# Optimization experiments

Measured on AMD Instinct MI355X. Metric: run time of the kernel, lower is better.

Reference implementation:

```python
import jax, jax.numpy as jnp
import numpy as np

# ---- neuron / simulation params (network.yaml analogue) ----
THETA = 10.0      # spike threshold
TAU_SR = 4.0      # SRM (psp) kernel time constant
TAU_REF = 4.0     # refractory kernel time constant
SCALE_REF = 2.0
TS = 1.0          # simulation step
T_SAMPLE = 1000
N_BATCH, N_IN, N_OUT = 16, 2048, 512
SPIKE_RATE = 0.1


def _alpha_kernel(tau, mult, eps_cut):
    # SLAYER _calculateAlphaKernel: truncated alpha function samples
    vals = []
    for t in np.arange(0.0, T_SAMPLE, TS):
        v = mult * t / tau * np.exp(1.0 - t / tau)
        if abs(v) < eps_cut and t > tau:
            break
        vals.append(v)
    return np.asarray(vals, dtype=np.float32)

SRM_KERNEL = _alpha_kernel(TAU_SR, 1.0, 0.01)
REF_KERNEL = _alpha_kernel(TAU_REF, -SCALE_REF * THETA, 0.0001)  # fullRefKernel=True
# pending-refractory shift vector: refKernel[0]==0 is consumed at spike time
REF_SHIFT = jnp.asarray(np.concatenate([REF_KERNEL[1:], [0.0]]).astype(np.float32))


def psp(spike_in):
    # causal temporal filter: psp[n,c,t] = Ts * sum_j srm[j] * s[n,c,t-j]
    N, C, T = spike_in.shape
    Ls = SRM_KERNEL.shape[0]
    x = spike_in.reshape(N * C, 1, T)
    k = jnp.asarray(SRM_KERNEL)[::-1].reshape(1, 1, Ls)  # flip -> convolution
    y = jax.lax.conv_general_dilated(
        x, k, window_strides=(1,), padding=[(Ls - 1, 0)],
        dimension_numbers=('NCH', 'OIH', 'NCH'))
    return y.reshape(N, C, T) * TS


def spike_scan(wpsp):
    # sequential spike generation with refractory feedback (SLAYER getSpikes)
    N, C, T = wpsp.shape
    L = REF_SHIFT.shape[0]

    def step(buf, x):
        u = x + buf[..., 0]                       # membrane incl. past refractory
        ind = (u >= THETA).astype(x.dtype)
        buf = jnp.concatenate([buf[..., 1:], jnp.zeros_like(buf[..., :1])], -1) \
              + ind[..., None] * REF_SHIFT        # schedule refractory for future t
        return buf, (ind / TS, u)

    buf0 = jnp.zeros((N, C, L), wpsp.dtype)
    _, (s, u) = jax.lax.scan(step, buf0, jnp.moveaxis(wpsp, -1, 0))
    return jnp.moveaxis(s, 0, -1), jnp.moveaxis(u, 0, -1)


def setup_inputs() -> dict:
    key = jax.random.key(0)
    k1, k2 = jax.random.split(key)
    spikeInput = (jax.random.uniform(k1, (N_BATCH, N_IN, T_SAMPLE)) < SPIKE_RATE
                  ).astype(jnp.float32)
    weight = jax.random.normal(k2, (N_OUT, N_IN), dtype=jnp.float32) * 0.3
    return {'spikeInput': spikeInput, 'weight': weight}


def reference(spikeInput, weight):
    p = psp(spikeInput)                           # [N, Nin, T]
    wpsp = jnp.einsum('oi,nit->not', weight, p)   # 1x1x1 conv == matmul, no bias
    spikes, _ = spike_scan(wpsp)                  # [N, Nout, T]
    return spikes
```

## Files before the change

### kernel.cpp

```cpp
#include <hip/hip_runtime.h>
#include <hip/hip_bf16.h>
#include <math.h>

#define NB 16
#define NIN 2048
#define NOUT 512
#define TT 1000
#define L_SRM 31

typedef int v4i  __attribute__((ext_vector_type(4)));
typedef int v16i __attribute__((ext_vector_type(16)));

__device__ __forceinline__ unsigned long long spread8(unsigned int b) {
    unsigned long long x = (unsigned long long)(b & 0xFFu) * 0x0101010101010101ULL;
    x &= 0x8040201008040201ULL;
    x |= x >> 4; x |= x >> 2; x |= x >> 1;
    return x & 0x0101010101010101ULL;
}

__global__ __launch_bounds__(256) void k_quant(const float* __restrict__ W,
                                               signed char* __restrict__ Bq) {
    int idx = blockIdx.x * 256 + threadIdx.x;
    int o = idx >> 11, i = idx & (NIN - 1);
    double w = (double)W[o * NIN + i];
    int wq = (int)rint(w * 536870912.0);
    int b0 = (int)(signed char)(wq & 255); int r = (wq - b0) >> 8;
    int b1 = (int)(signed char)(r  & 255); r = (r - b1) >> 8;
    int b2 = (int)(signed char)(r  & 255); r = (r - b2) >> 8;
    int b3 = r;
    size_t e = (size_t)o * NIN + i;
    Bq[e]                = (signed char)b0;
    Bq[e + 1048576]      = (signed char)b1;
    Bq[e + 2097152]      = (signed char)b2;
    Bq[e + 3145728]      = (signed char)b3;
}

__global__ __launch_bounds__(256) void k_extract(const float* __restrict__ s,
                                                 unsigned long long* __restrict__ bits) {
    __shared__ float tile[64][65];
    int tc = blockIdx.x, ic = blockIdx.y, n = blockIdx.z;
    int t0 = tc * 64, i0 = ic * 64;
    int tid = threadIdx.x;
    int r = tid >> 2, cq = tid & 3;
    const float* rp = s + ((size_t)(n * NIN + i0 + r)) * TT + t0;
    #pragma unroll
    for (int q = 0; q < 4; ++q) {
        int col = cq * 16 + q * 4;
        float4 v = make_float4(0.f, 0.f, 0.f, 0.f);
        if (t0 + col + 3 < TT) v = *(const float4*)(rp + col);
        tile[r][col] = v.x; tile[r][col + 1] = v.y;
        tile[r][col + 2] = v.z; tile[r][col + 3] = v.w;
    }
    __syncthreads();
    int lane = tid & 63, w = tid >> 6;
    #pragma unroll
    for (int k = 0; k < 16; ++k) {
        int tl = w * 16 + k;
        if (t0 + tl >= TT) break;
        unsigned long long m = __ballot(tile[lane][tl] != 0.0f);
        if (lane == 0) bits[((size_t)n * TT + t0 + tl) * 32 + ic] = m;
    }
}

__global__ __launch_bounds__(512) void k_spmm(const unsigned long long* __restrict__ bits,
                                              const signed char* __restrict__ Bq,
                                              double* __restrict__ z) {
    __shared__ char Alds[128 * 128];
    __shared__ char Blds[4][64 * 128];
    int tid = threadIdx.x;
    int bid = blockIdx.x;
    int o0  = (bid & 7) * 64;
    int nt0 = (bid >> 3) * 128;

    const int arow_w = tid >> 2, q = tid & 3;
    const int p_st = tid >> 7, orow = (tid >> 1) & 63, h = tid & 1;
    const unsigned int* agp = (const unsigned int*)bits + (size_t)(nt0 + arow_w) * 64 + q;
    const signed char*  bgp = Bq + (size_t)p_st * (NOUT * NIN)
                                 + (size_t)(o0 + orow) * NIN + h * 64;
    char* awp = Alds + arow_w * 128;
    const int xra_w = arow_w & 7;
    char* bwp = Blds[p_st] + orow * 128;
    const int xro_w = orow & 7;

    const int l = tid & 63, wv = tid >> 6;
    const int wm = wv >> 1, wn = wv & 1;
    const int arow = wm * 32 + (l & 31), xra = arow & 7;
    const int brow = wn * 32 + (l & 31), xrb = brow & 7;
    const int kg = l >> 5;

    v16i acc0 = {}, acc1 = {}, acc2 = {}, acc3 = {};

    unsigned int aw = agp[0];
    int4 bs0 = ((const int4*)bgp)[0], bs1 = ((const int4*)bgp)[1],
         bs2 = ((const int4*)bgp)[2], bs3 = ((const int4*)bgp)[3];

    for (int ks = 0; ks < 16; ++ks) {
        __syncthreads();
        {
            unsigned long long s0 = spread8(aw), s1 = spread8(aw >> 8),
                               s2 = spread8(aw >> 16), s3 = spread8(aw >> 24);
            ulonglong2 v0; v0.x = s0; v0.y = s1;
            ulonglong2 v1; v1.x = s2; v1.y = s3;
            *(ulonglong2*)(awp + (((2 * q)     ^ xra_w) << 4)) = v0;
            *(ulonglong2*)(awp + (((2 * q + 1) ^ xra_w) << 4)) = v1;
            *(int4*)(bwp + (((h * 4 + 0) ^ xro_w) << 4)) = bs0;
            *(int4*)(bwp + (((h * 4 + 1) ^ xro_w) << 4)) = bs1;
            *(int4*)(bwp + (((h * 4 + 2) ^ xro_w) << 4)) = bs2;
            *(int4*)(bwp + (((h * 4 + 3) ^ xro_w) << 4)) = bs3;
        }
        __syncthreads();
        if (ks < 15) {
            aw = agp[(ks + 1) * 4];
            const int4* g = (const int4*)(bgp + (size_t)(ks + 1) * 128);
            bs0 = g[0]; bs1 = g[1]; bs2 = g[2]; bs3 = g[3];
        }
        #pragma unroll
        for (int ksub = 0; ksub < 4; ++ksub) {
            int ca = ksub * 2 + kg;
            v4i av  = *(const v4i*)(Alds    + arow * 128 + (((ca) ^ xra) << 4));
            v4i bv0 = *(const v4i*)(Blds[0] + brow * 128 + (((ca) ^ xrb) << 4));
            v4i bv1 = *(const v4i*)(Blds[1] + brow * 128 + (((ca) ^ xrb) << 4));
            v4i bv2 = *(const v4i*)(Blds[2] + brow * 128 + (((ca) ^ xrb) << 4));
            v4i bv3 = *(const v4i*)(Blds[3] + brow * 128 + (((ca) ^ xrb) << 4));
            acc0 = __builtin_amdgcn_mfma_i32_32x32x32_i8(av, bv0, acc0, 0, 0, 0);
            acc1 = __builtin_amdgcn_mfma_i32_32x32x32_i8(av, bv1, acc1, 0, 0, 0);
            acc2 = __builtin_amdgcn_mfma_i32_32x32x32_i8(av, bv2, acc2, 0, 0, 0);
            acc3 = __builtin_amdgcn_mfma_i32_32x32x32_i8(av, bv3, acc3, 0, 0, 0);
        }
    }

    #pragma unroll
    for (int r = 0; r < 16; ++r) {
        int row = (r & 3) + 8 * (r >> 2) + 4 * kg;
        long long tot = ((long long)acc3[r] << 24) + ((long long)acc2[r] << 16)
                      + ((long long)acc1[r] << 8)  +  (long long)acc0[r];
        double zv = (double)tot * (1.0 / 536870912.0);
        __builtin_nontemporal_store(zv,
            &z[(size_t)(nt0 + wm * 32 + row) * NOUT + (o0 + wn * 32 + (l & 31))]);
    }
}

__global__ __launch_bounds__(128) void k_conv(const double* __restrict__ z,
                                              double* __restrict__ wpsp) {
    __shared__ float srm_s[32];
    __shared__ __align__(16) double zs[62 * 128];
    int tid = threadIdx.x;
    if (tid < L_SRM) {
        double t = (double)tid;
        srm_s[tid] = (float)((t / 4.0) * exp(1.0 - t / 4.0));
    }
    int tb = blockIdx.x * 32;
    int oc = blockIdx.y * 128;
    int n  = blockIdx.z;
    const double* zp = z + ((size_t)n * TT) * NOUT + oc;
    int wv = tid >> 6, lane = tid & 63;
    for (int r = wv; r < 62; r += 2) {
        int t = tb - 30 + r;
        if (t >= 0 && t < TT) {
            const double* src = zp + (size_t)t * NOUT + lane * 2;
            __builtin_amdgcn_global_load_lds(
                (const __attribute__((address_space(1))) void*)src,
                (__attribute__((address_space(3))) void*)(&zs[r * 128]),
                16, 0, 0);
        } else {
            double2 zero; zero.x = 0.0; zero.y = 0.0;
            *(double2*)(&zs[r * 128 + lane * 2]) = zero;
        }
    }
    asm volatile("s_waitcnt vmcnt(0)" ::: "memory");
    __syncthreads();
    for (int tl = 0; tl < 32; ++tl) {
        int t = tb + tl;
        if (t >= TT) break;
        double a0 = 0., a1 = 0., a2 = 0., a3 = 0.;
        #pragma unroll
        for (int jj = 0; jj < 28; jj += 4) {
            a0 += (double)srm_s[jj]     * zs[(tl + 30 - jj) * 128 + tid];
            a1 += (double)srm_s[jj + 1] * zs[(tl + 29 - jj) * 128 + tid];
            a2 += (double)srm_s[jj + 2] * zs[(tl + 28 - jj) * 128 + tid];
            a3 += (double)srm_s[jj + 3] * zs[(tl + 27 - jj) * 128 + tid];
        }
        a0 += (double)srm_s[28] * zs[(tl + 2) * 128 + tid];
        a1 += (double)srm_s[29] * zs[(tl + 1) * 128 + tid];
        a2 += (double)srm_s[30] * zs[(tl + 0) * 128 + tid];
        wpsp[((size_t)n * TT + t) * NOUT + oc + tid] = (a0 + a1) + (a2 + a3);
    }
}

__global__ __launch_bounds__(64) void k_scan(const double* __restrict__ wpsp,
                                             float* __restrict__ out) {
    __shared__ float  refTab[64];
    __shared__ double Tb[8][256];
    __shared__ __align__(16) double xbuf[2][33 * 64];
    __shared__ float  obuf[64 * 33];
    int lane = threadIdx.x;
    {
        double d = (double)lane;
        refTab[lane] = (lane == 0) ? 0.0f
                     : (float)(-20.0 * (d / 4.0) * exp(1.0 - d / 4.0));
    }
    __syncthreads();
    for (int e = lane; e < 2048; e += 64) {
        int k = e >> 8, m = e & 255;
        double s = 0.0;
        #pragma unroll
        for (int j = 0; j < 8; ++j) {
            int idx = 8 * k + j + 1;
            if (((m >> j) & 1) && idx <= 63) s += (double)refTab[idx];
        }
        Tb[k][m] = s;
    }

    int n  = blockIdx.x >> 3;
    int o0 = (blockIdx.x & 7) << 6;
    const double* wp = wpsp + ((size_t)n * TT) * NOUT + o0;
    float* op = out + ((size_t)(n * NOUT) + o0 + lane) * TT;

    int halfSel = lane >> 5;
    int colSel  = (lane & 31) * 2;
    #define STAGE(bf, tb, nrows)                                                   \
        for (int p = 0; p < (nrows) / 2; ++p) {                                    \
            const double* src = wp + (size_t)((tb) + 2 * p + halfSel) * NOUT + colSel; \
            __builtin_amdgcn_global_load_lds(                                      \
                (const __attribute__((address_space(1))) void*)src,                \
                (__attribute__((address_space(3))) void*)(&xbuf[bf][p * 128]),     \
                16, 0, 0);                                                         \
        }

    unsigned long long hist = 0ULL;
    bool sp = false;
    int buf = 0;
    STAGE(0, 0, 32);
    asm volatile("s_waitcnt vmcnt(0)" ::: "memory");
    __syncthreads();

    double x = xbuf[0][lane];
    double partial = 0.0;
    double c0 = 0.0, c1 = Tb[0][1];

    for (int tb = 0; tb < TT; tb += 32) {
        int nnext = TT - (tb + 32); if (nnext > 32) nnext = 32;
        if (nnext > 0) { STAGE(buf ^ 1, tb + 32, nnext); }
        #pragma unroll
        for (int tl = 0; tl < 32; ++tl) {
            hist = ((hist << 1) | (unsigned long long)sp) & 0x7FFFFFFFFFFFFFFFULL;
            unsigned long long hs = (hist << 1) & 0x7FFFFFFFFFFFFFFFULL;
            double T1 = Tb[1][(unsigned)((hs >>  8) & 255)];
            double T2 = Tb[2][(unsigned)((hs >> 16) & 255)];
            double T3 = Tb[3][(unsigned)((hs >> 24) & 255)];
            double T4 = Tb[4][(unsigned)((hs >> 32) & 255)];
            double T5 = Tb[5][(unsigned)((hs >> 40) & 255)];
            double T6 = Tb[6][(unsigned)((hs >> 48) & 255)];
            double T7 = Tb[7][(unsigned)((hs >> 56) & 255)];
            unsigned m = (unsigned)(hs & 255);
            double nc0 = Tb[0][m];
            double nc1 = Tb[0][m | 1];
            double nx  = xbuf[buf][(tl + 1) * 64 + lane];
            double u = (x + partial) + (sp ? c1 : c0);
            sp = (u >= 10.0);
            obuf[lane * 33 + tl] = sp ? 1.0f : 0.0f;
            partial = ((T1 + T2) + (T3 + T4)) + ((T5 + T6) + T7);
            c0 = nc0; c1 = nc1; x = nx;
        }
        int nrows = TT - tb; if (nrows > 32) nrows = 32;
        for (int k = 0; k + 3 < nrows; k += 4) {
            float4 v = make_float4(obuf[lane * 33 + k],     obuf[lane * 33 + k + 1],
                                   obuf[lane * 33 + k + 2], obuf[lane * 33 + k + 3]);
            *(float4*)(op + tb + k) = v;
        }
        asm volatile("s_waitcnt vmcnt(0)" ::: "memory");
        __syncthreads();
        buf ^= 1;
        x = xbuf[buf][lane];
    }
    #undef STAGE
}

extern "C" void kernel_launch(void* const* d_in, const int* in_sizes, int n_in,
                              void* d_out, int out_size, void* d_ws, size_t ws_size,
                              hipStream_t stream) {
    const float* spikeInput = (const float*)d_in[0];
    const float* weight     = (const float*)d_in[1];
    float* out = (float*)d_out;

    char* ws = (char*)d_ws;
    unsigned long long* bits = (unsigned long long*)ws;
    signed char*        Bq   = (signed char*)(ws + 4194304);
    double*             z    = (double*)(ws + 8388608);
    double*             wpsp = (double*)(ws + 73924608);

    k_quant<<<(NOUT * NIN) / 256, 256, 0, stream>>>(weight, Bq);
    k_extract<<<dim3(16, 32, 16), 256, 0, stream>>>(spikeInput, bits);
    k_spmm<<<1000, 512, 0, stream>>>(bits, Bq, z);
    k_conv<<<dim3(32, 4, 16), 128, 0, stream>>>(z, wpsp);
    k_scan<<<128, 64, 0, stream>>>(wpsp, out);
}
```

Before: 485.6 us.

## Pipeline spike scan recurrence two steps ahead to shorten critical path

The sequential spike-scan loop now computes refractory partial sums and the next membrane input one step further ahead. This leaves only an add, a compare and a select on the per-timestep dependency chain, which the serial scan is bound by. The lookup-table entries for the next step are fetched as paired double2 loads, and the input staging buffer grows by one row to allow the deeper lookahead. The cost is more live registers and more complex state hand-off at each 32-step block boundary, which could introduce correctness or occupancy problems.

```diff
diff --git a/kernel.cpp b/kernel.cpp
--- a/kernel.cpp
+++ b/kernel.cpp
@@ -191,7 +191,7 @@
                                              float* __restrict__ out) {
     __shared__ float  refTab[64];
     __shared__ double Tb[8][256];
-    __shared__ __align__(16) double xbuf[2][33 * 64];
+    __shared__ __align__(16) double xbuf[2][34 * 64];
     __shared__ float  obuf[64 * 33];
     int lane = threadIdx.x;
     {
@@ -215,6 +215,7 @@
     int o0 = (blockIdx.x & 7) << 6;
     const double* wp = wpsp + ((size_t)n * TT) * NOUT + o0;
     float* op = out + ((size_t)(n * NOUT) + o0 + lane) * TT;
+    const double* Tb0 = &Tb[0][0];
 
     int halfSel = lane >> 5;
     int colSel  = (lane & 31) * 2;
@@ -227,40 +228,51 @@
                 16, 0, 0);                                                         \
         }
 
-    unsigned long long hist = 0ULL;
-    bool sp = false;
     int buf = 0;
     STAGE(0, 0, 32);
     asm volatile("s_waitcnt vmcnt(0)" ::: "memory");
     __syncthreads();
 
-    double x = xbuf[0][lane];
-    double partial = 0.0;
-    double c0 = 0.0, c1 = Tb[0][1];
+    unsigned long long h = 0ULL;
+    bool sp1 = false;
+    double xp = xbuf[0][lane];
+    double x1 = xbuf[0][64 + lane];
+    double partial1 = 0.0;
+    double p0 = 0., p1 = 0., p2 = 0., p3 = 0., p4 = 0., p5 = 0., p6 = 0.;
+    double e0 = 0.0, e1 = 0.0;
+    double c1_0 = Tb0[0], c1_1 = Tb0[1], c1_2 = Tb0[2], c1_3 = Tb0[3];
 
     for (int tb = 0; tb < TT; tb += 32) {
         int nnext = TT - (tb + 32); if (nnext > 32) nnext = 32;
         if (nnext > 0) { STAGE(buf ^ 1, tb + 32, nnext); }
         #pragma unroll
         for (int tl = 0; tl < 32; ++tl) {
-            hist = ((hist << 1) | (unsigned long long)sp) & 0x7FFFFFFFFFFFFFFFULL;
-            unsigned long long hs = (hist << 1) & 0x7FFFFFFFFFFFFFFFULL;
-            double T1 = Tb[1][(unsigned)((hs >>  8) & 255)];
-            double T2 = Tb[2][(unsigned)((hs >> 16) & 255)];
-            double T3 = Tb[3][(unsigned)((hs >> 24) & 255)];
-            double T4 = Tb[4][(unsigned)((hs >> 32) & 255)];
-            double T5 = Tb[5][(unsigned)((hs >> 40) & 255)];
-            double T6 = Tb[6][(unsigned)((hs >> 48) & 255)];
-            double T7 = Tb[7][(unsigned)((hs >> 56) & 255)];
+            h = (h << 1) | (unsigned long long)sp1;
+            unsigned long long hs = h << 2;
+            double q1 = Tb[1][(unsigned)((hs >>  8) & 255)];
+            double q2 = Tb[2][(unsigned)((hs >> 16) & 255)];
+            double q3 = Tb[3][(unsigned)((hs >> 24) & 255)];
+            double q4 = Tb[4][(unsigned)((hs >> 32) & 255)];
+            double q5 = Tb[5][(unsigned)((hs >> 40) & 255)];
+            double q6 = Tb[6][(unsigned)((hs >> 48) & 255)];
+            double q7 = Tb[7][(unsigned)((hs >> 56) & 255)];
             unsigned m = (unsigned)(hs & 255);
-            double nc0 = Tb[0][m];
-            double nc1 = Tb[0][m | 1];
-            double nx  = xbuf[buf][(tl + 1) * 64 + lane];
-            double u = (x + partial) + (sp ? c1 : c0);
-            sp = (u >= 10.0);
-            obuf[lane * 33 + tl] = sp ? 1.0f : 0.0f;
-            partial = ((T1 + T2) + (T3 + T4)) + ((T5 + T6) + T7);
-            c0 = nc0; c1 = nc1; x = nx;
+            double2 nc01 = *(const double2*)(Tb0 + m);
+            double2 nc23 = *(const double2*)(Tb0 + m + 2);
+            double nx = xbuf[buf][(tl + 2) * 64 + lane];
+            double e0n = sp1 ? c1_2 : c1_0;
+            double e1n = sp1 ? c1_3 : c1_1;
+            double np1 = ((p0 + p1) + (p2 + p3)) + ((p4 + p5) + p6);
+            double u = xp + (sp1 ? e1 : e0);
+            bool spt = (u >= 10.0);
+            obuf[lane * 33 + tl] = spt ? 1.0f : 0.0f;
+            double nxp = x1 + np1;
+            sp1 = spt;
+            e0 = e0n; e1 = e1n;
+            partial1 = np1;
+            xp = nxp; x1 = nx;
+            p0 = q1; p1 = q2; p2 = q3; p3 = q4; p4 = q5; p5 = q6; p6 = q7;
+            c1_0 = nc01.x; c1_1 = nc01.y; c1_2 = nc23.x; c1_3 = nc23.y;
         }
         int nrows = TT - tb; if (nrows > 32) nrows = 32;
         for (int k = 0; k + 3 < nrows; k += 4) {
@@ -271,7 +283,8 @@
         asm volatile("s_waitcnt vmcnt(0)" ::: "memory");
         __syncthreads();
         buf ^= 1;
-        x = xbuf[buf][lane];
+        xp = xbuf[buf][lane] + partial1;
+        x1 = xbuf[buf][64 + lane];
     }
     #undef STAGE
 }
```

Result: no change. 481.7 us (-0.8%).
